# Kernel tuning notes

Measured on AMD Instinct MI355X. Metric: run time of the kernel, lower is better.

## Reference

```python
import jax, jax.numpy as jnp
import numpy as np

N_NODES = 50000
N_EDGES = 800000
D_FEAT = 96
D_HID = 10
N_GRAPHS = 512


def setup_inputs() -> dict:
    key = jax.random.key(0)
    ks = jax.random.split(key, 8)
    x = jax.random.normal(ks[0], (N_NODES, D_FEAT), dtype=jnp.float32)
    edge_index = jax.random.randint(ks[1], (2, N_EDGES), 0, N_NODES, dtype=jnp.int64)
    edge_attr = jax.random.uniform(ks[2], (N_EDGES,), dtype=jnp.float32)
    batch = jnp.sort(jax.random.randint(ks[3], (N_NODES,), 0, N_GRAPHS, dtype=jnp.int64))
    W1 = jax.random.normal(ks[4], (D_FEAT, D_HID), dtype=jnp.float32) / np.sqrt(D_FEAT)
    b1 = jax.random.normal(ks[5], (D_HID,), dtype=jnp.float32) * 0.01
    W2 = jax.random.normal(ks[6], (D_HID, 1), dtype=jnp.float32) / np.sqrt(D_HID)
    b2 = jax.random.normal(ks[7], (1,), dtype=jnp.float32) * 0.01
    return {"x": x, "edge_index": edge_index, "edge_attr": edge_attr,
            "batch": batch, "W1": W1, "b1": b1, "W2": W2, "b2": b2}


def reference(x, edge_index, edge_attr, batch, W1, b1, W2, b2):
    src, dst = edge_index[0], edge_index[1]
    # SimpleConv (sum aggr, edge_attr as edge weight): out[i] = sum_{j->i} w_e * x[j]
    msgs = x[src] * edge_attr[:, None]                       # [E, D]
    h = jax.ops.segment_sum(msgs, dst, num_segments=N_NODES)  # [N, D]
    # global_mean_pool over batch index
    sums = jax.ops.segment_sum(h, batch, num_segments=N_GRAPHS)         # [G, D]
    counts = jax.ops.segment_sum(jnp.ones((N_NODES,), h.dtype), batch,
                                 num_segments=N_GRAPHS)
    pooled = sums / jnp.maximum(counts, 1.0)[:, None]
    z = jax.nn.relu(pooled)
    z = jax.nn.relu(z @ W1 + b1)
    return z @ W2 + b2                                        # [G, 1]
```

## Files before the change

kernel.cpp:

```cpp
#include <hip/hip_runtime.h>

#define NGRAPH 512
#define DF     96
#define DHID   10
#define NCHUNK 256
#define NBINS  4096
#define ECHMAX 3200
#define HTHR   1024
#define NTHR   256

static __device__ __forceinline__ unsigned short f2bf(float f) {
    unsigned int u = __float_as_uint(f);
    u = (u + 0x7fffu + ((u >> 16) & 1u)) >> 16;
    return (unsigned short)u;
}
static __device__ __forceinline__ float bf2f(unsigned short s) {
    return __uint_as_float(((unsigned int)s) << 16);
}
static __device__ __forceinline__ unsigned short f2h(float f) {
    _Float16 h = (_Float16)f;
    unsigned short u;
    __builtin_memcpy(&u, &h, 2);
    return u;
}
static __device__ __forceinline__ float h2f(unsigned short u) {
    _Float16 h;
    __builtin_memcpy(&h, &u, 2);
    return (float)h;
}

__global__ __launch_bounds__(HTHR) void sort_kernel(
    const int* __restrict__ edge_index,
    const float* __restrict__ edge_attr,
    const int* __restrict__ batch,
    const float* __restrict__ x,
    int E, int N, int echunk, unsigned int M,
    unsigned short* __restrict__ localpre,
    unsigned short* __restrict__ xb,
    unsigned int* __restrict__ ed)
{
    __shared__ int            lh[NBINS];
    __shared__ unsigned short sbin[ECHMAX];
    __shared__ unsigned int   sval[ECHMAX];
    __shared__ int            wvsum[16];

    const int blk = blockIdx.x, t = threadIdx.x;
    const int lane = t & 63, wv = t >> 6;

    const int nf4 = N * DF / 4;
    for (int i = blk * HTHR + t; i < nf4; i += NCHUNK * HTHR) {
        const float4 v = ((const float4*)x)[i];
        ushort4 o;
        o.x = f2bf(v.x); o.y = f2bf(v.y); o.z = f2bf(v.z); o.w = f2bf(v.w);
        ((ushort4*)xb)[i] = o;
    }

    for (int i = t; i < NBINS; i += HTHR) lh[i] = 0;
    __syncthreads();

    const int* __restrict__ src = edge_index;
    const int* __restrict__ dst = edge_index + E;
    const int lo = blk * echunk;
    const int hi = min(E, lo + echunk);
    for (int e = lo + t; e < hi; e += HTHR) {
        const int g = batch[dst[e]];
        const int r = (int)__umulhi((unsigned int)src[e], M);
        const int b = (g << 3) | r;
        sbin[e - lo] = (unsigned short)b;
        sval[e - lo] = (unsigned int)(src[e] & 0xffff)
                     | ((unsigned int)f2h(edge_attr[e]) << 16);
        atomicAdd(&lh[b], 1);
    }
    __syncthreads();

    const int v0 = lh[4 * t], v1 = lh[4 * t + 1],
              v2 = lh[4 * t + 2], v3 = lh[4 * t + 3];
    const int s = v0 + v1 + v2 + v3;
    int p = s;
#pragma unroll
    for (int d = 1; d < 64; d <<= 1) {
        const int u = __shfl_up(p, d, 64);
        if (lane >= d) p += u;
    }
    if (lane == 63) wvsum[wv] = p;
    __syncthreads();
    int add = 0;
#pragma unroll
    for (int i = 0; i < 16; ++i) if (i < wv) add += wvsum[i];
    const int ex = p - s + add;

    ushort4 o;
    o.x = (unsigned short)ex;
    o.y = (unsigned short)(ex + v0);
    o.z = (unsigned short)(ex + v0 + v1);
    o.w = (unsigned short)(ex + v0 + v1 + v2);
    ((ushort4*)(localpre + (size_t)blk * NBINS))[t] = o;
    __syncthreads();
    lh[4 * t]     = ex;
    lh[4 * t + 1] = ex + v0;
    lh[4 * t + 2] = ex + v0 + v1;
    lh[4 * t + 3] = ex + v0 + v1 + v2;
    __syncthreads();

    for (int e = lo + t; e < hi; e += HTHR) {
        const int i = e - lo;
        const int ppos = atomicAdd(&lh[sbin[i]], 1);
        ed[lo + ppos] = sval[i];
    }
}

__global__ __launch_bounds__(NTHR) void aggregate_kernel(
    const unsigned int* __restrict__ ed,
    const unsigned short* __restrict__ localpre,
    const unsigned short* __restrict__ xb,
    int E, int echunk,
    float* __restrict__ partial)
{
    __shared__ int   starts[NCHUNK];
    __shared__ int   cum[NCHUNK];
    __shared__ int   wt[4];
    __shared__ int   sT;
    __shared__ float sh4[4][DF];

    const int bin = blockIdx.x, t = threadIdx.x;
    const int lane = t & 63, wv = t >> 6;

    const int pb = (int)localpre[(size_t)t * NBINS + bin];
    const int pe = (bin < NBINS - 1)
                 ? (int)localpre[(size_t)t * NBINS + bin + 1]
                 : (min(echunk, E - t * echunk));
    const int cnt = pe - pb;
    starts[t] = t * echunk + pb;

    int p = cnt;
#pragma unroll
    for (int d = 1; d < 64; d <<= 1) {
        const int u = __shfl_up(p, d, 64);
        if (lane >= d) p += u;
    }
    if (lane == 63) wt[wv] = p;
    __syncthreads();
    int add = 0;
#pragma unroll
    for (int i = 0; i < 4; ++i) if (i < wv) add += wt[i];
    const int incl = p + add;
    cum[t] = incl - cnt;
    if (t == NTHR - 1) sT = incl;
    __syncthreads();
    const int T = sT;

    const int eg = lane >> 3;
    const int fc = lane & 7;
    float acc[12];
#pragma unroll
    for (int i = 0; i < 12; ++i) acc[i] = 0.f;

    for (int k = wv * 8 + eg; k < T; k += 32) {
        int lo2 = 0, hi2 = NCHUNK - 1;
#pragma unroll
        for (int it = 0; it < 8; ++it) {
            const int m = (lo2 + hi2 + 1) >> 1;
            if (cum[m] <= k) lo2 = m; else hi2 = m - 1;
        }
        const unsigned int sw = ed[starts[lo2] + (k - cum[lo2])];
        const float w = h2f((unsigned short)(sw >> 16));
        const ushort4* __restrict__ row =
            (const ushort4*)xb + (size_t)(sw & 0xffffu) * 24;
#pragma unroll
        for (int c = 0; c < 3; ++c) {
            const ushort4 vv = row[fc + c * 8];
            acc[c * 4 + 0] += w * bf2f(vv.x);
            acc[c * 4 + 1] += w * bf2f(vv.y);
            acc[c * 4 + 2] += w * bf2f(vv.z);
            acc[c * 4 + 3] += w * bf2f(vv.w);
        }
    }

#pragma unroll
    for (int m = 8; m <= 32; m <<= 1) {
#pragma unroll
        for (int i = 0; i < 12; ++i) acc[i] += __shfl_xor(acc[i], m, 64);
    }
    if (eg == 0) {
#pragma unroll
        for (int c = 0; c < 3; ++c)
#pragma unroll
            for (int k2 = 0; k2 < 4; ++k2)
                sh4[wv][c * 32 + fc * 4 + k2] = acc[c * 4 + k2];
    }
    __syncthreads();
    if (t < DF)
        partial[(size_t)bin * DF + t] =
            sh4[0][t] + sh4[1][t] + sh4[2][t] + sh4[3][t];
}

__global__ __launch_bounds__(128) void finish_kernel(
    const float* __restrict__ partial,
    const int* __restrict__ batch,
    int N,
    const float* __restrict__ W1,
    const float* __restrict__ b1,
    const float* __restrict__ W2,
    const float* __restrict__ b2,
    float* __restrict__ out)
{
    __shared__ float sW1[DF * DHID];
    __shared__ float fin[DF];
    __shared__ int   scnt[2];
    const int g = blockIdx.x, t = threadIdx.x;

    if (t < 2) {
        const int key = g + t;
        int lo = 0, hi = N;
        while (lo < hi) {
            const int m = (lo + hi) >> 1;
            if (batch[m] < key) lo = m + 1; else hi = m;
        }
        scnt[t] = lo;
    }
    for (int i = t; i < DF * DHID; i += 128) sW1[i] = W1[i];
    __syncthreads();

    if (t < DF) {
        float s = 0.f;
#pragma unroll
        for (int r = 0; r < 8; ++r)
            s += partial[(size_t)((g << 3) | r) * DF + t];
        const int cnt = scnt[1] - scnt[0];
        fin[t] = fmaxf(s / fmaxf((float)cnt, 1.f), 0.f);
    }
    __syncthreads();
    if (t < 16) {
        float v = 0.f;
        if (t < DHID) {
            float h = b1[t];
            for (int f = 0; f < DF; ++f) h += fin[f] * sW1[f * DHID + t];
            v = fmaxf(h, 0.f) * W2[t];
        }
#pragma unroll
        for (int m = 1; m < 16; m <<= 1) v += __shfl_xor(v, m, 16);
        if (t == 0) out[g] = v + b2[0];
    }
}

extern "C" void kernel_launch(void* const* d_in, const int* in_sizes, int n_in,
                              void* d_out, int out_size, void* d_ws, size_t ws_size,
                              hipStream_t stream) {
    const float* x          = (const float*)d_in[0];
    const int*   edge_index = (const int*)  d_in[1];
    const float* edge_attr  = (const float*)d_in[2];
    const int*   batch      = (const int*)  d_in[3];
    const float* W1         = (const float*)d_in[4];
    const float* b1         = (const float*)d_in[5];
    const float* W2         = (const float*)d_in[6];
    const float* b2         = (const float*)d_in[7];

    const int E = in_sizes[1] / 2;
    const int N = in_sizes[3];
    const int echunk = (E + NCHUNK - 1) / NCHUNK;
    const unsigned int RDIV = (unsigned int)((N + 7) / 8);
    const unsigned int M = (unsigned int)((0x100000000ULL + RDIV - 1) / RDIV);

    char* ws = (char*)d_ws;
    unsigned int*   ed = (unsigned int*)ws;
    unsigned short* xb = (unsigned short*)(ws + (size_t)4 * E);
    char* tail = ws + (size_t)4 * E + (size_t)2 * N * DF;
    tail = (char*)(((size_t)tail + 255) & ~(size_t)255);
    unsigned short* localpre = (unsigned short*)tail;
    float*          partial  = (float*)(localpre + (size_t)NCHUNK * NBINS);

    sort_kernel<<<NCHUNK, HTHR, 0, stream>>>(edge_index, edge_attr, batch, x,
                                             E, N, echunk, M,
                                             localpre, xb, ed);
    aggregate_kernel<<<NBINS, NTHR, 0, stream>>>(ed, localpre, xb,
                                                 E, echunk, partial);
    finish_kernel<<<NGRAPH, 128, 0, stream>>>(partial, batch, N,
                                              W1, b1, W2, b2, (float*)d_out);
}
```

Baseline: 56.26 us.

## Stage sorted edges in shared memory and walk chunk segments directly in aggregate

The sort kernel now scatters edges into a shared-memory buffer by bin and then writes them to global memory in contiguous order, replacing scattered global stores with coalesced ones. The aggregate kernel drops the block-wide prefix scan and the per-edge binary search over chunk offsets. Each wave instead loops over its quarter of the chunks and processes each chunk's segment in groups of eight edges. This costs extra shared memory in the sort kernel and can leave lanes idle, and waves unevenly loaded, when segments are short or empty.

```diff
diff --git a/kernel.cpp b/kernel.cpp
--- a/kernel.cpp
+++ b/kernel.cpp
@@ -42,6 +42,7 @@
     __shared__ int            lh[NBINS];
     __shared__ unsigned short sbin[ECHMAX];
     __shared__ unsigned int   sval[ECHMAX];
+    __shared__ unsigned int   sval2[ECHMAX];
     __shared__ int            wvsum[16];
 
     const int blk = blockIdx.x, t = threadIdx.x;
@@ -102,11 +103,15 @@
     lh[4 * t + 3] = ex + v0 + v1 + v2;
     __syncthreads();
 
-    for (int e = lo + t; e < hi; e += HTHR) {
-        const int i = e - lo;
+    const int cnt = hi - lo;
+    for (int i = t; i < cnt; i += HTHR) {
         const int ppos = atomicAdd(&lh[sbin[i]], 1);
-        ed[lo + ppos] = sval[i];
-    }
+        sval2[ppos] = sval[i];
+    }
+    __syncthreads();
+
+    for (int j = t; j < cnt; j += HTHR)
+        ed[lo + j] = sval2[j];
 }
 
 __global__ __launch_bounds__(NTHR) void aggregate_kernel(
@@ -116,38 +121,22 @@
     int E, int echunk,
     float* __restrict__ partial)
 {
-    __shared__ int   starts[NCHUNK];
-    __shared__ int   cum[NCHUNK];
-    __shared__ int   wt[4];
-    __shared__ int   sT;
-    __shared__ float sh4[4][DF];
+    __shared__ int            sstart[NCHUNK];
+    __shared__ unsigned short slen[NCHUNK];
+    __shared__ float          sh4[4][DF];
 
     const int bin = blockIdx.x, t = threadIdx.x;
     const int lane = t & 63, wv = t >> 6;
 
-    const int pb = (int)localpre[(size_t)t * NBINS + bin];
-    const int pe = (bin < NBINS - 1)
-                 ? (int)localpre[(size_t)t * NBINS + bin + 1]
-                 : (min(echunk, E - t * echunk));
-    const int cnt = pe - pb;
-    starts[t] = t * echunk + pb;
-
-    int p = cnt;
-#pragma unroll
-    for (int d = 1; d < 64; d <<= 1) {
-        const int u = __shfl_up(p, d, 64);
-        if (lane >= d) p += u;
-    }
-    if (lane == 63) wt[wv] = p;
-    __syncthreads();
-    int add = 0;
-#pragma unroll
-    for (int i = 0; i < 4; ++i) if (i < wv) add += wt[i];
-    const int incl = p + add;
-    cum[t] = incl - cnt;
-    if (t == NTHR - 1) sT = incl;
-    __syncthreads();
-    const int T = sT;
+    {
+        const int pb = (int)localpre[(size_t)t * NBINS + bin];
+        const int pe = (bin < NBINS - 1)
+                     ? (int)localpre[(size_t)t * NBINS + bin + 1]
+                     : (min(echunk, E - t * echunk));
+        sstart[t] = t * echunk + pb;
+        slen[t]   = (unsigned short)(pe - pb);
+    }
+    __syncthreads();
 
     const int eg = lane >> 3;
     const int fc = lane & 7;
@@ -155,25 +144,28 @@
 #pragma unroll
     for (int i = 0; i < 12; ++i) acc[i] = 0.f;
 
-    for (int k = wv * 8 + eg; k < T; k += 32) {
-        int lo2 = 0, hi2 = NCHUNK - 1;
-#pragma unroll
-        for (int it = 0; it < 8; ++it) {
-            const int m = (lo2 + hi2 + 1) >> 1;
-            if (cum[m] <= k) lo2 = m; else hi2 = m - 1;
+    const int c0 = wv * (NCHUNK / 4);
+    for (int c = c0; c < c0 + (NCHUNK / 4); ++c) {
+        const int n = (int)slen[c];
+        if (n == 0) continue;
+        const int st = sstart[c];
+        for (int base = 0; base < n; base += 8) {
+            const int k = base + eg;
+            if (k < n) {
+                const unsigned int sw = ed[st + k];
+                const float w = h2f((unsigned short)(sw >> 16));
+                const ushort4* __restrict__ row =
+                    (const ushort4*)xb + (size_t)(sw & 0xffffu) * 24;
+#pragma unroll
+                for (int cc = 0; cc < 3; ++cc) {
+                    const ushort4 vv = row[fc + cc * 8];
+                    acc[cc * 4 + 0] += w * bf2f(vv.x);
+                    acc[cc * 4 + 1] += w * bf2f(vv.y);
+                    acc[cc * 4 + 2] += w * bf2f(vv.z);
+                    acc[cc * 4 + 3] += w * bf2f(vv.w);
+                }
+            }
         }
-        const unsigned int sw = ed[starts[lo2] + (k - cum[lo2])];
-        const float w = h2f((unsigned short)(sw >> 16));
-        const ushort4* __restrict__ row =
-            (const ushort4*)xb + (size_t)(sw & 0xffffu) * 24;
-#pragma unroll
-        for (int c = 0; c < 3; ++c) {
-            const ushort4 vv = row[fc + c * 8];
-            acc[c * 4 + 0] += w * bf2f(vv.x);
-            acc[c * 4 + 1] += w * bf2f(vv.y);
-            acc[c * 4 + 2] += w * bf2f(vv.z);
-            acc[c * 4 + 3] += w * bf2f(vv.w);
-        }
     }
 
 #pragma unroll
@@ -183,10 +175,10 @@
     }
     if (eg == 0) {
 #pragma unroll
-        for (int c = 0; c < 3; ++c)
+        for (int cc = 0; cc < 3; ++cc)
 #pragma unroll
             for (int k2 = 0; k2 < 4; ++k2)
-                sh4[wv][c * 32 + fc * 4 + k2] = acc[c * 4 + k2];
+                sh4[wv][cc * 32 + fc * 4 + k2] = acc[cc * 4 + k2];
     }
     __syncthreads();
     if (t < DF)
```

Result: slower. 105.5 us (+87.5%).

## Stage sorted edges in LDS and precompute per-bin edge index table

Applied to the files above, without the earlier changes.

The sort kernel now scatters each chunk's edges into a shared-memory buffer and then writes them to global memory contiguously, in place of scattering atomically-placed writes straight to global. The aggregate kernel builds a shared table mapping each bin-local edge slot to its global position, replacing the per-edge 8-step binary search over chunk offsets for the first 2048 edges; a fallback loop keeps the binary search for any overflow. This adds 12.8 KB of LDS to the sort kernel and a serial per-thread fill loop in aggregate, which may reduce occupancy or add latency.

```diff
diff --git a/kernel.cpp b/kernel.cpp
--- a/kernel.cpp
+++ b/kernel.cpp
@@ -6,6 +6,7 @@
 #define NCHUNK 256
 #define NBINS  4096
 #define ECHMAX 3200
+#define EIDXMAX 2048
 #define HTHR   1024
 #define NTHR   256
 
@@ -42,6 +43,7 @@
     __shared__ int            lh[NBINS];
     __shared__ unsigned short sbin[ECHMAX];
     __shared__ unsigned int   sval[ECHMAX];
+    __shared__ unsigned int   sval2[ECHMAX];
     __shared__ int            wvsum[16];
 
     const int blk = blockIdx.x, t = threadIdx.x;
@@ -102,11 +104,15 @@
     lh[4 * t + 3] = ex + v0 + v1 + v2;
     __syncthreads();
 
-    for (int e = lo + t; e < hi; e += HTHR) {
-        const int i = e - lo;
+    const int cnt = hi - lo;
+    for (int i = t; i < cnt; i += HTHR) {
         const int ppos = atomicAdd(&lh[sbin[i]], 1);
-        ed[lo + ppos] = sval[i];
-    }
+        sval2[ppos] = sval[i];
+    }
+    __syncthreads();
+
+    for (int j = t; j < cnt; j += HTHR)
+        ed[lo + j] = sval2[j];
 }
 
 __global__ __launch_bounds__(NTHR) void aggregate_kernel(
@@ -116,8 +122,9 @@
     int E, int echunk,
     float* __restrict__ partial)
 {
-    __shared__ int   starts[NCHUNK];
+    __shared__ int   eidx[EIDXMAX];
     __shared__ int   cum[NCHUNK];
+    __shared__ int   sstart[NCHUNK];
     __shared__ int   wt[4];
     __shared__ int   sT;
     __shared__ float sh4[4][DF];
@@ -130,7 +137,8 @@
                  ? (int)localpre[(size_t)t * NBINS + bin + 1]
                  : (min(echunk, E - t * echunk));
     const int cnt = pe - pb;
-    starts[t] = t * echunk + pb;
+    const int start = t * echunk + pb;
+    sstart[t] = start;
 
     int p = cnt;
 #pragma unroll
@@ -144,10 +152,17 @@
 #pragma unroll
     for (int i = 0; i < 4; ++i) if (i < wv) add += wt[i];
     const int incl = p + add;
-    cum[t] = incl - cnt;
+    const int base0 = incl - cnt;
+    cum[t] = base0;
     if (t == NTHR - 1) sT = incl;
     __syncthreads();
     const int T = sT;
+
+    for (int j = 0; j < cnt; ++j) {
+        const int idx = base0 + j;
+        if (idx < EIDXMAX) eidx[idx] = start + j;
+    }
+    __syncthreads();
 
     const int eg = lane >> 3;
     const int fc = lane & 7;
@@ -155,14 +170,29 @@
 #pragma unroll
     for (int i = 0; i < 12; ++i) acc[i] = 0.f;
 
-    for (int k = wv * 8 + eg; k < T; k += 32) {
+    const int Tc = min(T, EIDXMAX);
+    for (int k = wv * 8 + eg; k < Tc; k += 32) {
+        const unsigned int sw = ed[eidx[k]];
+        const float w = h2f((unsigned short)(sw >> 16));
+        const ushort4* __restrict__ row =
+            (const ushort4*)xb + (size_t)(sw & 0xffffu) * 24;
+#pragma unroll
+        for (int c = 0; c < 3; ++c) {
+            const ushort4 vv = row[fc + c * 8];
+            acc[c * 4 + 0] += w * bf2f(vv.x);
+            acc[c * 4 + 1] += w * bf2f(vv.y);
+            acc[c * 4 + 2] += w * bf2f(vv.z);
+            acc[c * 4 + 3] += w * bf2f(vv.w);
+        }
+    }
+    for (int k = EIDXMAX + wv * 8 + eg; k < T; k += 32) {
         int lo2 = 0, hi2 = NCHUNK - 1;
 #pragma unroll
         for (int it = 0; it < 8; ++it) {
             const int m = (lo2 + hi2 + 1) >> 1;
             if (cum[m] <= k) lo2 = m; else hi2 = m - 1;
         }
-        const unsigned int sw = ed[starts[lo2] + (k - cum[lo2])];
+        const unsigned int sw = ed[sstart[lo2] + (k - cum[lo2])];
         const float w = h2f((unsigned short)(sw >> 16));
         const ushort4* __restrict__ row =
             (const ushort4*)xb + (size_t)(sw & 0xffffu) * 24;
```

Measured after the change: 50.07 us. 11.0% less time.
